# Performance work log

Measured on AMD Instinct MI355X. Metric: run time of the kernel, lower is better.

## Reference

```python
import jax, jax.numpy as jnp
import numpy as np

T, B, D = 2048, 32, 1024
AH, H = 128, 8
N, N2 = D // H, AH // H


def setup_inputs() -> dict:
    key = jax.random.key(0)
    ks = jax.random.split(key, 7)
    s1 = 1.0 / np.sqrt(N)
    s2 = 1.0 / np.sqrt(N2)
    return {
        "hyp": jax.random.normal(ks[0], (T, B, D), dtype=jnp.float32),
        "W_w": jax.random.uniform(ks[1], (N2, N), jnp.float32, -s1, s1),
        "W_b": jax.random.uniform(ks[2], (N2,), jnp.float32, -s1, s1),
        "Wm_w": jax.random.uniform(ks[3], (N2, N), jnp.float32, -s1, s1),
        "Wm_b": jax.random.uniform(ks[4], (N2,), jnp.float32, -s1, s1),
        "Wh_w": jax.random.uniform(ks[5], (1, N2), jnp.float32, -s2, s2),
        "Wh_b": jax.random.uniform(ks[6], (1,), jnp.float32, -s2, s2),
        "dan_hidden_size": D,
        "attention_hidden_size": AH,
        "multihead_size": H,
    }


def reference(hyp, W_w, W_b, Wm_w, Wm_b, Wh_w, Wh_b,
              dan_hidden_size, attention_hidden_size, multihead_size):
    t, b, d = hyp.shape
    h_ = multihead_size
    n = d // h_
    # (T,B,D) -> (B,H,T,N); weights are shared across heads in the original loop
    x = jnp.transpose(hyp.reshape(t, b, h_, n), (1, 2, 0, 3))
    m = x.mean(axis=2, keepdims=True)                      # (B,H,1,N) mean over time
    gate_x = jnp.tanh(jnp.einsum('bhtn,kn->bhtk', x, W_w) + W_b)
    gate_m = jnp.tanh(jnp.einsum('bhtn,kn->bhtk', m, Wm_w) + Wm_b)
    hgate = gate_x * gate_m                                 # (B,H,T,N2)
    logits = jnp.einsum('bhtk,ok->bhto', hgate, Wh_w) + Wh_b  # (B,H,T,1)
    a = jax.nn.softmax(logits, axis=2)                      # softmax over time
    c = jnp.sum(a * x, axis=2)                              # (B,H,N)
    return c.reshape(b, h_ * n)
```

## Files before the change

kernel.cpp:

```cpp
#include <hip/hip_runtime.h>
#include <hip/hip_fp16.h>
#include <math.h>

#define T_   2048
#define B_   32
#define D_   1024
#define H_   8
#define N_   128
#define NK   16
#define TSPL 8
#define TBLK (T_/TSPL)
#define BD4  (B_*D_/4)
#define APS  132
#define LOG2E 1.4426950408889634f

typedef __attribute__((ext_vector_type(8))) short short8;
typedef __attribute__((ext_vector_type(4))) float f32x4;

__device__ __forceinline__ void split_bf16(float4 a, float4 b,
                                           short8& hi, short8& lo) {
    union { uint32_t u[4]; short8 v; } H, L;
    uint32_t x0 = __float_as_uint(a.x), x1 = __float_as_uint(a.y);
    uint32_t x2 = __float_as_uint(a.z), x3 = __float_as_uint(a.w);
    uint32_t x4 = __float_as_uint(b.x), x5 = __float_as_uint(b.y);
    uint32_t x6 = __float_as_uint(b.z), x7 = __float_as_uint(b.w);
    H.u[0] = (x0 >> 16) | (x1 & 0xFFFF0000u);
    H.u[1] = (x2 >> 16) | (x3 & 0xFFFF0000u);
    H.u[2] = (x4 >> 16) | (x5 & 0xFFFF0000u);
    H.u[3] = (x6 >> 16) | (x7 & 0xFFFF0000u);
    float l0 = a.x - __uint_as_float(x0 & 0xFFFF0000u);
    float l1 = a.y - __uint_as_float(x1 & 0xFFFF0000u);
    float l2 = a.z - __uint_as_float(x2 & 0xFFFF0000u);
    float l3 = a.w - __uint_as_float(x3 & 0xFFFF0000u);
    float l4 = b.x - __uint_as_float(x4 & 0xFFFF0000u);
    float l5 = b.y - __uint_as_float(x5 & 0xFFFF0000u);
    float l6 = b.z - __uint_as_float(x6 & 0xFFFF0000u);
    float l7 = b.w - __uint_as_float(x7 & 0xFFFF0000u);
    L.u[0] = (__float_as_uint(l0) >> 16) | (__float_as_uint(l1) & 0xFFFF0000u);
    L.u[1] = (__float_as_uint(l2) >> 16) | (__float_as_uint(l3) & 0xFFFF0000u);
    L.u[2] = (__float_as_uint(l4) >> 16) | (__float_as_uint(l5) & 0xFFFF0000u);
    L.u[3] = (__float_as_uint(l6) >> 16) | (__float_as_uint(l7) & 0xFFFF0000u);
    hi = H.v; lo = L.v;
}

__device__ __forceinline__ float tanh_fast(float d) {
    return 1.f - 2.f * __frcp_rn(exp2f(d * (2.f * LOG2E)) + 1.f);
}

#define LOADX(dst, step_) { \
    const int trow_ = t0 + (step_) * 64 + w * 16 + kk; \
    const size_t rb_ = (size_t)trow_ * BD4 + base4; \
    (dst)[0] = hyp4[rb_ + g * 2];      (dst)[1] = hyp4[rb_ + g * 2 + 1]; \
    (dst)[2] = hyp4[rb_ + 8 + g * 2];  (dst)[3] = hyp4[rb_ + 8 + g * 2 + 1]; \
    (dst)[4] = hyp4[rb_ + 16 + g * 2]; (dst)[5] = hyp4[rb_ + 16 + g * 2 + 1]; \
    (dst)[6] = hyp4[rb_ + 24 + g * 2]; (dst)[7] = hyp4[rb_ + 24 + g * 2 + 1]; }

__global__ __launch_bounds__(256, 4) void k_p(const float* __restrict__ hyp,
                                              const float* __restrict__ Ww,
                                              const float* __restrict__ Wb,
                                              float* __restrict__ part,
                                              __half* __restrict__ Pbuf) {
    __shared__ float red[4 * N_];
    __shared__ __half Pl[TBLK * NK];
    const int tid  = threadIdx.x;
    const int lane = tid & 63;
    const int w    = tid >> 6;
    const int blk  = blockIdx.x;
    const int bh   = blk >> 3;
    const int spl  = blk & 7;
    const int b = bh >> 3, h = bh & 7;
    const int t0 = spl * TBLK;
    const float4* hyp4 = (const float4*)hyp;
    const float4* Ww4  = (const float4*)Ww;
    const int base4 = b * (D_ / 4) + h * (N_ / 4);
    const int kk = lane & 15;
    const int g  = lane >> 4;

    short8 wh[4], wlo[4];
#pragma unroll
    for (int ks = 0; ks < 4; ++ks) {
        float4 wa  = Ww4[kk * 32 + ks * 8 + g * 2];
        float4 wb4 = Ww4[kk * 32 + ks * 8 + g * 2 + 1];
        split_bf16(wa, wb4, wh[ks], wlo[ks]);
    }
    const float wbr = Wb[kk];

    float4 cs[8];
#pragma unroll
    for (int m = 0; m < 8; ++m) cs[m] = make_float4(0.f, 0.f, 0.f, 0.f);

#pragma unroll
    for (int step = 0; step < 4; ++step) {
        float4 xq[8];
        LOADX(xq, step);
#pragma unroll
        for (int m = 0; m < 8; ++m) {
            cs[m].x += xq[m].x; cs[m].y += xq[m].y;
            cs[m].z += xq[m].z; cs[m].w += xq[m].w;
        }
        f32x4 acc = {0.f, 0.f, 0.f, 0.f};
#pragma unroll
        for (int ks = 0; ks < 4; ++ks) {
            short8 xh, xl;
            split_bf16(xq[2*ks], xq[2*ks+1], xh, xl);
            acc = __builtin_amdgcn_mfma_f32_16x16x32_bf16(xh, wh[ks],  acc, 0, 0, 0);
            acc = __builtin_amdgcn_mfma_f32_16x16x32_bf16(xl, wh[ks],  acc, 0, 0, 0);
            acc = __builtin_amdgcn_mfma_f32_16x16x32_bf16(xh, wlo[ks], acc, 0, 0, 0);
        }
        const int tl = step * 64 + w * 16 + g * 4;
#pragma unroll
        for (int i = 0; i < 4; ++i)
            Pl[(tl + i) * NK + kk] = __float2half(tanh_fast(acc[i] + wbr));
    }
    __syncthreads();
    {
        const uint4* src = (const uint4*)Pl;
        uint4* dst = (uint4*)(Pbuf + ((size_t)bh * T_ + t0) * NK);
        dst[tid]       = src[tid];
        dst[tid + 256] = src[tid + 256];
    }
#pragma unroll
    for (int m = 0; m < 8; ++m) {
#pragma unroll
        for (int mask = 1; mask <= 8; mask <<= 1) {
            cs[m].x += __shfl_xor(cs[m].x, mask, 64);
            cs[m].y += __shfl_xor(cs[m].y, mask, 64);
            cs[m].z += __shfl_xor(cs[m].z, mask, 64);
            cs[m].w += __shfl_xor(cs[m].w, mask, 64);
        }
    }
    if (kk == 0) {
#pragma unroll
        for (int m = 0; m < 8; ++m) {
            int nb = 32 * (m >> 1) + 8 * g + 4 * (m & 1);
            red[w * N_ + nb + 0] = cs[m].x;
            red[w * N_ + nb + 1] = cs[m].y;
            red[w * N_ + nb + 2] = cs[m].z;
            red[w * N_ + nb + 3] = cs[m].w;
        }
    }
    __syncthreads();
    if (tid < N_)
        part[blk * N_ + tid] = (red[tid] + red[N_ + tid])
                             + (red[2*N_ + tid] + red[3*N_ + tid]);
}

__global__ __launch_bounds__(256, 4) void k_att(const float* __restrict__ hyp,
                                                const float* __restrict__ part,
                                                const float* __restrict__ Wmw,
                                                const float* __restrict__ Wmb,
                                                const float* __restrict__ Whw,
                                                const __half* __restrict__ Pbuf,
                                                float* __restrict__ attp) {
    __shared__ float red[4 * N_];
    __shared__ float zred[4];
    __shared__ float m_l[N_];
    __shared__ float gw_l[NK];
    const int tid  = threadIdx.x;
    const int lane = tid & 63;
    const int w    = tid >> 6;
    const int j    = (int)blockIdx.x;
    const int blk  = (j & 7) + 8 * (255 - (j >> 3));
    const int bh   = blk >> 3;
    const int spl  = blk & 7;
    const int b = bh >> 3, h = bh & 7;
    const int t0 = spl * TBLK;
    const float4* hyp4 = (const float4*)hyp;
    const int base4 = b * (D_ / 4) + h * (N_ / 4);
    const int kk = lane & 15;
    const int g  = lane >> 4;

    if (tid < N_) {
        float s = 0.f;
#pragma unroll
        for (int s8 = 0; s8 < TSPL; ++s8) s += part[(bh * TSPL + s8) * N_ + tid];
        m_l[tid] = s * (1.f / (float)T_);
    }
    __syncthreads();
    if (tid < N_) {
        int k = tid >> 3, g3 = tid & 7;
        float dsum = 0.f;
#pragma unroll
        for (int i = 0; i < 16; ++i) {
            int n = g3 * 16 + i;
            dsum = fmaf(m_l[n], Wmw[k * N_ + n], dsum);
        }
        dsum += __shfl_xor(dsum, 1, 64);
        dsum += __shfl_xor(dsum, 2, 64);
        dsum += __shfl_xor(dsum, 4, 64);
        if (g3 == 0) gw_l[k] = tanhf(dsum + Wmb[k]) * Whw[k];
    }
    __syncthreads();
    float gmv[NK];
#pragma unroll
    for (int jq = 0; jq < NK; ++jq) gmv[jq] = gw_l[jq];

    float4 cacc[8];
#pragma unroll
    for (int m = 0; m < 8; ++m) cacc[m] = make_float4(0.f, 0.f, 0.f, 0.f);
    float zacc = 0.f;

#pragma unroll
    for (int step = 0; step < 4; ++step) {
        const int tr = t0 + step * 64 + w * 16 + kk;
        union { uint4 u; __half2 h[8]; } P0, P1;
        const uint4* pv = (const uint4*)(Pbuf + (size_t)(bh * T_ + tr) * NK);
        P0.u = pv[0]; P1.u = pv[1];
        float4 xq[8];
        LOADX(xq, step);
        float lg = 0.f;
#pragma unroll
        for (int q = 0; q < 4; ++q) {
            float2 f0 = __half22float2(P0.h[q]);
            float2 f1 = __half22float2(P1.h[q]);
            lg = fmaf(f0.x, gmv[2*q + 0], lg);
            lg = fmaf(f0.y, gmv[2*q + 1], lg);
            lg = fmaf(f1.x, gmv[8 + 2*q + 0], lg);
            lg = fmaf(f1.y, gmv[8 + 2*q + 1], lg);
        }
        float e = exp2f(lg * LOG2E);
        zacc += e;
#pragma unroll
        for (int m = 0; m < 8; ++m) {
            cacc[m].x = fmaf(e, xq[m].x, cacc[m].x);
            cacc[m].y = fmaf(e, xq[m].y, cacc[m].y);
            cacc[m].z = fmaf(e, xq[m].z, cacc[m].z);
            cacc[m].w = fmaf(e, xq[m].w, cacc[m].w);
        }
    }
#pragma unroll
    for (int m = 0; m < 8; ++m) {
#pragma unroll
        for (int mask = 1; mask <= 8; mask <<= 1) {
            cacc[m].x += __shfl_xor(cacc[m].x, mask, 64);
            cacc[m].y += __shfl_xor(cacc[m].y, mask, 64);
            cacc[m].z += __shfl_xor(cacc[m].z, mask, 64);
            cacc[m].w += __shfl_xor(cacc[m].w, mask, 64);
        }
    }
    float z = zacc;
    z += __shfl_xor(z, 1, 64);
    z += __shfl_xor(z, 2, 64);
    z += __shfl_xor(z, 4, 64);
    z += __shfl_xor(z, 8, 64);
    if (kk == 0) {
#pragma unroll
        for (int m = 0; m < 8; ++m) {
            int nb = 32 * (m >> 1) + 8 * g + 4 * (m & 1);
            red[w * N_ + nb + 0] = cacc[m].x;
            red[w * N_ + nb + 1] = cacc[m].y;
            red[w * N_ + nb + 2] = cacc[m].z;
            red[w * N_ + nb + 3] = cacc[m].w;
        }
    }
    if (lane == 0) zred[w] = z;
    __syncthreads();
    if (tid < N_) {
        attp[(size_t)blk * APS + tid] =
            (red[tid] + red[N_ + tid]) + (red[2*N_ + tid] + red[3*N_ + tid]);
    } else if (tid == N_) {
        attp[(size_t)blk * APS + N_] =
            (zred[0] + zred[1]) + (zred[2] + zred[3]);
    }
}

__global__ __launch_bounds__(128) void k_red(const float* __restrict__ attp,
                                             float* __restrict__ out) {
    int bh = blockIdx.x, tid = threadIdx.x;
    float Z = 0.f, c = 0.f;
#pragma unroll
    for (int s = 0; s < TSPL; ++s) {
        const float* pp = &attp[(size_t)(bh * TSPL + s) * APS];
        Z += pp[N_];
        c += pp[tid];
    }
    out[bh * N_ + tid] = c / Z;
}

extern "C" void kernel_launch(void* const* d_in, const int* in_sizes, int n_in,
                              void* d_out, int out_size, void* d_ws, size_t ws_size,
                              hipStream_t stream) {
    const float* hyp = (const float*)d_in[0];
    const float* Ww  = (const float*)d_in[1];
    const float* Wb  = (const float*)d_in[2];
    const float* Wmw = (const float*)d_in[3];
    const float* Wmb = (const float*)d_in[4];
    const float* Whw = (const float*)d_in[5];
    float* out  = (float*)d_out;
    float* part = (float*)d_ws;
    float* attp = part + 2048 * N_;
    __half* Pbuf = (__half*)((char*)d_ws + (4 << 20));

    k_p  <<<dim3(B_ * H_ * TSPL), 256, 0, stream>>>(hyp, Ww, Wb, part, Pbuf);
    k_att<<<dim3(B_ * H_ * TSPL), 256, 0, stream>>>(hyp, part, Wmw, Wmb, Whw,
                                                    Pbuf, attp);
    k_red<<<dim3(B_ * H_), 128, 0, stream>>>(attp, out);
}
```

Baseline: 105.4 us.

## Fuse final reduction into attention kernel via last-block atomic counter

Removes the separate k_red launch by having each attention block atomically bump a per-(b,h) counter. The last block to finish then sums the eight split partials and writes the normalized output. The counter is reset inside k_p. The P buffer is also written and read with nontemporal stores and loads to avoid cache pollution. This saves a kernel launch and its tail, but adds atomics and relies on correct memory ordering across blocks.

```diff
diff --git a/kernel.cpp b/kernel.cpp
--- a/kernel.cpp
+++ b/kernel.cpp
@@ -16,6 +16,7 @@
 
 typedef __attribute__((ext_vector_type(8))) short short8;
 typedef __attribute__((ext_vector_type(4))) float f32x4;
+typedef __attribute__((ext_vector_type(4))) unsigned int uint4v;
 
 __device__ __forceinline__ void split_bf16(float4 a, float4 b,
                                            short8& hi, short8& lo) {
@@ -59,7 +60,8 @@
                                               const float* __restrict__ Ww,
                                               const float* __restrict__ Wb,
                                               float* __restrict__ part,
-                                              __half* __restrict__ Pbuf) {
+                                              __half* __restrict__ Pbuf,
+                                              int* __restrict__ counter) {
     __shared__ float red[4 * N_];
     __shared__ __half Pl[TBLK * NK];
     const int tid  = threadIdx.x;
@@ -76,6 +78,8 @@
     const int kk = lane & 15;
     const int g  = lane >> 4;
 
+    if (spl == 0 && tid == 0) counter[bh] = 0;
+
     short8 wh[4], wlo[4];
 #pragma unroll
     for (int ks = 0; ks < 4; ++ks) {
@@ -114,10 +118,10 @@
     }
     __syncthreads();
     {
-        const uint4* src = (const uint4*)Pl;
-        uint4* dst = (uint4*)(Pbuf + ((size_t)bh * T_ + t0) * NK);
-        dst[tid]       = src[tid];
-        dst[tid + 256] = src[tid + 256];
+        const uint4v* src = (const uint4v*)Pl;
+        uint4v* dst = (uint4v*)(Pbuf + ((size_t)bh * T_ + t0) * NK);
+        __builtin_nontemporal_store(src[tid],       &dst[tid]);
+        __builtin_nontemporal_store(src[tid + 256], &dst[tid + 256]);
     }
 #pragma unroll
     for (int m = 0; m < 8; ++m) {
@@ -151,11 +155,14 @@
                                                 const float* __restrict__ Wmb,
                                                 const float* __restrict__ Whw,
                                                 const __half* __restrict__ Pbuf,
-                                                float* __restrict__ attp) {
+                                                float* __restrict__ attp,
+                                                int* __restrict__ counter,
+                                                float* __restrict__ out) {
     __shared__ float red[4 * N_];
     __shared__ float zred[4];
     __shared__ float m_l[N_];
     __shared__ float gw_l[NK];
+    __shared__ int last_s;
     const int tid  = threadIdx.x;
     const int lane = tid & 63;
     const int w    = tid >> 6;
@@ -203,9 +210,10 @@
 #pragma unroll
     for (int step = 0; step < 4; ++step) {
         const int tr = t0 + step * 64 + w * 16 + kk;
-        union { uint4 u; __half2 h[8]; } P0, P1;
-        const uint4* pv = (const uint4*)(Pbuf + (size_t)(bh * T_ + tr) * NK);
-        P0.u = pv[0]; P1.u = pv[1];
+        union { uint4v u; __half2 h[8]; } P0, P1;
+        const uint4v* pv = (const uint4v*)(Pbuf + (size_t)(bh * T_ + tr) * NK);
+        P0.u = __builtin_nontemporal_load(pv);
+        P1.u = __builtin_nontemporal_load(pv + 1);
         float4 xq[8];
         LOADX(xq, step);
         float lg = 0.f;
@@ -256,25 +264,34 @@
     if (lane == 0) zred[w] = z;
     __syncthreads();
     if (tid < N_) {
-        attp[(size_t)blk * APS + tid] =
-            (red[tid] + red[N_ + tid]) + (red[2*N_ + tid] + red[3*N_ + tid]);
+        float v = (red[tid] + red[N_ + tid]) + (red[2*N_ + tid] + red[3*N_ + tid]);
+        __hip_atomic_store(&attp[(size_t)blk * APS + tid], v,
+                           __ATOMIC_RELAXED, __HIP_MEMORY_SCOPE_AGENT);
     } else if (tid == N_) {
-        attp[(size_t)blk * APS + N_] =
-            (zred[0] + zred[1]) + (zred[2] + zred[3]);
-    }
-}
-
-__global__ __launch_bounds__(128) void k_red(const float* __restrict__ attp,
-                                             float* __restrict__ out) {
-    int bh = blockIdx.x, tid = threadIdx.x;
-    float Z = 0.f, c = 0.f;
-#pragma unroll
-    for (int s = 0; s < TSPL; ++s) {
-        const float* pp = &attp[(size_t)(bh * TSPL + s) * APS];
-        Z += pp[N_];
-        c += pp[tid];
-    }
-    out[bh * N_ + tid] = c / Z;
+        float zz = (zred[0] + zred[1]) + (zred[2] + zred[3]);
+        __hip_atomic_store(&attp[(size_t)blk * APS + N_], zz,
+                           __ATOMIC_RELAXED, __HIP_MEMORY_SCOPE_AGENT);
+    }
+    __syncthreads();
+    if (tid == 0) {
+        int old = __hip_atomic_fetch_add(&counter[bh], 1,
+                                         __ATOMIC_ACQ_REL, __HIP_MEMORY_SCOPE_AGENT);
+        last_s = (old == TSPL - 1);
+    }
+    __syncthreads();
+    if (last_s && tid < N_) {
+        float Z = 0.f, c = 0.f;
+#pragma unroll
+        for (int s = 0; s < TSPL; ++s) {
+            const float* pp = &attp[(size_t)(bh * TSPL + s) * APS];
+            float zz = __hip_atomic_load(&pp[N_], __ATOMIC_RELAXED,
+                                         __HIP_MEMORY_SCOPE_AGENT);
+            float cc = __hip_atomic_load(&pp[tid], __ATOMIC_RELAXED,
+                                         __HIP_MEMORY_SCOPE_AGENT);
+            Z += zz; c += cc;
+        }
+        out[bh * N_ + tid] = c / Z;
+    }
 }
 
 extern "C" void kernel_launch(void* const* d_in, const int* in_sizes, int n_in,
@@ -289,10 +306,11 @@
     float* out  = (float*)d_out;
     float* part = (float*)d_ws;
     float* attp = part + 2048 * N_;
+    int*   counter = (int*)(attp + 2048 * APS);
     __half* Pbuf = (__half*)((char*)d_ws + (4 << 20));
 
-    k_p  <<<dim3(B_ * H_ * TSPL), 256, 0, stream>>>(hyp, Ww, Wb, part, Pbuf);
+    k_p  <<<dim3(B_ * H_ * TSPL), 256, 0, stream>>>(hyp, Ww, Wb, part, Pbuf,
+                                                    counter);
     k_att<<<dim3(B_ * H_ * TSPL), 256, 0, stream>>>(hyp, part, Wmw, Wmb, Whw,
-                                                    Pbuf, attp);
-    k_red<<<dim3(B_ * H_), 128, 0, stream>>>(attp, out);
-}
+                                                    Pbuf, attp, counter, out);
+}
```

New measurement: 173.2 us. 64.4% more time.
